# Kernel optimization log

Hardware: AMD Instinct MI355X
Metric: run time of the kernel (lower is better)

## Reference

```python
import jax, jax.numpy as jnp
import numpy as np

N_NODES = 50000
N_EDGES = 800000
NODE_IN, EDGE_IN, EFT, OUT = 128, 64, 32, 64


def setup_inputs() -> dict:
    key = jax.random.key(0)
    ks = jax.random.split(key, 8)
    h = jax.random.normal(ks[0], (N_NODES, NODE_IN), dtype=jnp.float32)
    edge_feat = jax.random.normal(ks[1], (N_EDGES, EDGE_IN), dtype=jnp.float32)
    src = jax.random.randint(ks[2], (N_EDGES,), 0, N_NODES, dtype=jnp.int32)
    dst = jax.random.randint(ks[3], (N_EDGES,), 0, N_NODES, dtype=jnp.int32)
    Wn = jax.random.normal(ks[4], (OUT, NODE_IN), dtype=jnp.float32) * 0.05
    We = jax.random.normal(ks[5], (EFT, EDGE_IN), dtype=jnp.float32) * 0.05
    Wa = jax.random.normal(ks[6], (1, OUT + EFT + OUT), dtype=jnp.float32) * 0.05
    W2 = jax.random.normal(ks[7], (OUT, OUT + EFT), dtype=jnp.float32) * 0.05
    return {"h": h, "edge_feat": edge_feat, "src": src, "dst": dst,
            "Wn": Wn, "We": We, "Wa": Wa, "W2": W2}


def reference(h, edge_feat, src, dst, Wn, We, Wa, W2):
    N = h.shape[0]
    # node / edge feature projections (bias=False linears)
    z = h @ Wn.T                       # [N, OUT]
    ef = edge_feat @ We.T              # [E, EFT]
    # per-edge message: concat(src node ft, edge ft)
    zne = jnp.concatenate([z[src], ef], axis=1)            # [E, OUT+EFT]
    # attention logit: leaky_relu(attn_fc([zne, z_dst]))
    a = jnp.concatenate([zne, z[dst]], axis=1) @ Wa.T      # [E, 1]
    s = jax.nn.leaky_relu(a[:, 0], negative_slope=0.01)    # [E]
    # segment softmax over incoming edges of each dst node
    seg_max = jax.ops.segment_max(s, dst, num_segments=N)
    ex = jnp.exp(s - seg_max[dst])
    denom = jax.ops.segment_sum(ex, dst, num_segments=N)
    alpha = ex / denom[dst]                                # [E]
    # weighted scatter-sum aggregation, then fc2
    agg = jax.ops.segment_sum(alpha[:, None] * zne, dst, num_segments=N)
    h_new = agg @ W2.T                                     # [N, OUT]
    # DGL semantics: nodes with no incoming messages keep ndata['z'] = fc_n(h)
    deg = jax.ops.segment_sum(jnp.ones_like(s), dst, num_segments=N)
    return jnp.where((deg > 0)[:, None], h_new, z)
```

## Files before the change

### kernel.cpp

```cpp
#include <hip/hip_runtime.h>
#include <hip/hip_bf16.h>
#include <math.h>

#define N_NODES 50000
#define N_EDGES 800000
#define NB1 196

typedef __attribute__((ext_vector_type(8))) short bf16x8;
typedef __attribute__((ext_vector_type(4))) float f32x4;

__device__ __forceinline__ unsigned short f2bf(float f) {
    union { __hip_bfloat16 b; unsigned short u; } cv;
    cv.b = __float2bfloat16(f);
    return cv.u;
}
__device__ __forceinline__ float bf2f(unsigned short u) {
    return __uint_as_float(((unsigned)u) << 16);
}
__device__ __forceinline__ unsigned pack2bf(float a, float b) {
    return (unsigned)f2bf(a) | ((unsigned)f2bf(b) << 16);
}
union BFU { bf16x8 v; unsigned u[4]; };

__global__ __launch_bounds__(256) void kw_kernel(const float* __restrict__ We,
                                                 const float* __restrict__ Wa,
                                                 const float* __restrict__ Wn,
                                                 const float* __restrict__ W2,
                                                 short* __restrict__ Bpack,
                                                 int* __restrict__ degi) {
    int t = blockIdx.x * 256 + threadIdx.x;
    if (t < N_NODES) degi[t] = 0;
    if (t < 34 * 512) {
        int f = t >> 9, u = t & 511, lane = u >> 3, j = u & 7;
        int c = lane & 15, G = lane >> 4;
        float v = 0.f;
        if (f < 8) {
            int s = f >> 2, n = f & 3;
            int kp = 32 * s + 8 * G + j;
            #pragma unroll
            for (int kk = 0; kk < 32; ++kk)
                v += W2[(16 * n + c) * 96 + 64 + kk] * We[kk * 64 + kp];
        } else if (f < 10) {
            int s = f - 8;
            if (c == 0) {
                int kp = 32 * s + 8 * G + j;
                #pragma unroll
                for (int jj = 0; jj < 32; ++jj) v += Wa[64 + jj] * We[jj * 64 + kp];
            }
        } else if (f < 26) {
            int qf = f - 10, s = qf >> 2, n = qf & 3;
            v = Wn[(16 * n + c) * 128 + 32 * s + 8 * G + j];
        } else {
            int qf = f - 26, s = qf >> 2, n = qf & 3;
            v = W2[(16 * n + c) * 96 + 32 * s + 8 * G + j];
        }
        Bpack[t] = (short)f2bf(v);
    }
}

__global__ __launch_bounds__(256) void node_hist_kernel(
    const float* __restrict__ h, const float* __restrict__ Wa,
    const short* __restrict__ Bpack, const int* __restrict__ dst,
    float* __restrict__ z, ushort4* __restrict__ y16p,
    float* __restrict__ asrc, float* __restrict__ adst,
    int* __restrict__ degi, int* __restrict__ ranks)
{
    __shared__ float zl[4][1088];
    int t = threadIdx.x;
    if (blockIdx.x >= 782) {
        int e = (blockIdx.x - 782) * 256 + t;
        if (e < N_EDGES) ranks[e] = atomicAdd(&degi[dst[e]], 1);
        return;
    }
    int w = t >> 6, l = t & 63, c = l & 15, G = l >> 4;
    int T = blockIdx.x * 4 + w;
    if (T >= 3125) return;
    int n0 = T * 16;
    const bf16x8* Bp = (const bf16x8*)Bpack;

    const float* hp = h + (size_t)(n0 + c) * 128 + 8 * G;
    bf16x8 a[4];
    #pragma unroll
    for (int s = 0; s < 4; ++s) {
        float4 lo = *(const float4*)(hp + 32 * s);
        float4 hi = *(const float4*)(hp + 32 * s + 4);
        BFU ua;
        ua.u[0] = pack2bf(lo.x, lo.y);
        ua.u[1] = pack2bf(lo.z, lo.w);
        ua.u[2] = pack2bf(hi.x, hi.y);
        ua.u[3] = pack2bf(hi.z, hi.w);
        a[s] = ua.v;
    }
    f32x4 acc[4] = {{0.f,0.f,0.f,0.f},{0.f,0.f,0.f,0.f},{0.f,0.f,0.f,0.f},{0.f,0.f,0.f,0.f}};
    #pragma unroll
    for (int n = 0; n < 4; ++n)
        #pragma unroll
        for (int s = 0; s < 4; ++s)
            acc[n] = __builtin_amdgcn_mfma_f32_16x16x32_bf16(a[s], Bp[(10 + 4*s + n)*64 + l], acc[n], 0, 0, 0);

    float was[4], wad[4];
    #pragma unroll
    for (int n = 0; n < 4; ++n) { was[n] = Wa[16*n + c]; wad[n] = Wa[96 + 16*n + c]; }

    #pragma unroll
    for (int r = 0; r < 4; ++r) {
        int row = n0 + 4 * G + r;
        #pragma unroll
        for (int n = 0; n < 4; ++n) {
            z[(size_t)row * 64 + 16 * n + c] = acc[n][r];
            zl[w][(4 * G + r) * 68 + 16 * n + c] = acc[n][r];
        }
        float ps = acc[0][r]*was[0] + acc[1][r]*was[1] + acc[2][r]*was[2] + acc[3][r]*was[3];
        float pd = acc[0][r]*wad[0] + acc[1][r]*wad[1] + acc[2][r]*wad[2] + acc[3][r]*wad[3];
        ps += __shfl_xor(ps, 1); ps += __shfl_xor(ps, 2);
        ps += __shfl_xor(ps, 4); ps += __shfl_xor(ps, 8);
        pd += __shfl_xor(pd, 1); pd += __shfl_xor(pd, 2);
        pd += __shfl_xor(pd, 4); pd += __shfl_xor(pd, 8);
        if (c == 0) { asrc[row] = ps; adst[row] = pd; }
    }

    bf16x8 ay[2];
    #pragma unroll
    for (int s = 0; s < 2; ++s) {
        BFU ua;
        #pragma unroll
        for (int jp = 0; jp < 4; ++jp)
            ua.u[jp] = pack2bf(zl[w][c * 68 + 32 * s + 8 * G + 2 * jp],
                               zl[w][c * 68 + 32 * s + 8 * G + 2 * jp + 1]);
        ay[s] = ua.v;
    }
    f32x4 accy[4] = {{0.f,0.f,0.f,0.f},{0.f,0.f,0.f,0.f},{0.f,0.f,0.f,0.f},{0.f,0.f,0.f,0.f}};
    #pragma unroll
    for (int n = 0; n < 4; ++n)
        #pragma unroll
        for (int s = 0; s < 2; ++s)
            accy[n] = __builtin_amdgcn_mfma_f32_16x16x32_bf16(ay[s], Bp[(26 + 4*s + n)*64 + l], accy[n], 0, 0, 0);
    #pragma unroll
    for (int r = 0; r < 4; ++r) {
        ushort4 yo;
        yo.x = f2bf(accy[0][r]); yo.y = f2bf(accy[1][r]);
        yo.z = f2bf(accy[2][r]); yo.w = f2bf(accy[3][r]);
        y16p[(size_t)(n0 + 4 * G + r) * 16 + c] = yo;
    }
}

__global__ __launch_bounds__(256) void scan1_kernel(const int* __restrict__ degi,
                                                    int* __restrict__ partial) {
    int t = threadIdx.x, i = blockIdx.x * 256 + t;
    int d = (i < N_NODES) ? degi[i] : 0;
    #pragma unroll
    for (int off = 32; off; off >>= 1) d += __shfl_down(d, off);
    __shared__ int wsum[4];
    if ((t & 63) == 0) wsum[t >> 6] = d;
    __syncthreads();
    if (t == 0) partial[blockIdx.x] = wsum[0] + wsum[1] + wsum[2] + wsum[3];
}

__global__ __launch_bounds__(256) void scan2_kernel(int* __restrict__ partial) {
    __shared__ int s[256];
    int t = threadIdx.x;
    int v = (t < NB1) ? partial[t] : 0;
    s[t] = v; __syncthreads();
    for (int off = 1; off < 256; off <<= 1) {
        int x = (t >= off) ? s[t - off] : 0;
        __syncthreads();
        s[t] += x;
        __syncthreads();
    }
    if (t < NB1) partial[t] = s[t] - v;
}

__global__ __launch_bounds__(256) void scan3_kernel(const int* __restrict__ degi,
                                                    const int* __restrict__ partial,
                                                    int* __restrict__ start) {
    __shared__ int s[256];
    int t = threadIdx.x, i = blockIdx.x * 256 + t;
    int d = (i < N_NODES) ? degi[i] : 0;
    s[t] = d; __syncthreads();
    for (int off = 1; off < 256; off <<= 1) {
        int x = (t >= off) ? s[t - off] : 0;
        __syncthreads();
        s[t] += x;
        __syncthreads();
    }
    if (i < N_NODES) start[i] = partial[blockIdx.x] + s[t] - d;
}

__global__ __launch_bounds__(256, 2) void edge_kernel(
    const float* __restrict__ edge_feat, const int* __restrict__ src,
    const int* __restrict__ dst, const int* __restrict__ ranks,
    const int* __restrict__ start, const float* __restrict__ asrc,
    const float* __restrict__ adst, const short* __restrict__ Bpack,
    const ushort4* __restrict__ y16p,
    unsigned short* __restrict__ wout, float* __restrict__ exslot)
{
    int t = threadIdx.x, w = t >> 6, l = t & 63;
    int c = l & 15, G = l >> 4;
    int wbase = blockIdx.x * 256 + w * 64;

    const bf16x8* Bp = (const bf16x8*)Bpack;
    bf16x8 bc[8];
    #pragma unroll
    for (int f = 0; f < 8; ++f) bc[f] = Bp[f * 64 + l];
    bf16x8 b2a = Bp[8 * 64 + l];
    bf16x8 b2b = Bp[9 * 64 + l];

    int e = wbase + l;
    int se = src[e];
    int de = dst[e];
    int slot = start[de] + ranks[e];
    float apre = asrc[se] + adst[de];

    const float* efr = edge_feat + (size_t)(wbase + c) * 64 + G * 8;
    float4 n0 = *(const float4*)(efr);
    float4 n1 = *(const float4*)(efr + 4);
    float4 n2 = *(const float4*)(efr + 32);
    float4 n3 = *(const float4*)(efr + 36);

    #pragma unroll
    for (int k = 0; k < 4; ++k) {
        float4 c0 = n0, c1 = n1, c2 = n2, c3 = n3;
        if (k < 3) {
            const float* efn = edge_feat + (size_t)(wbase + 16 * (k + 1) + c) * 64 + G * 8;
            n0 = *(const float4*)(efn);
            n1 = *(const float4*)(efn + 4);
            n2 = *(const float4*)(efn + 32);
            n3 = *(const float4*)(efn + 36);
        }
        int sr[4], sl4[4]; float ap[4];
        #pragma unroll
        for (int r = 0; r < 4; ++r) {
            int si = 16 * k + 4 * G + r;
            sr[r]  = __shfl(se, si);
            sl4[r] = __shfl(slot, si);
            ap[r]  = __shfl(apre, si);
        }
        ushort4 yv[4];
        #pragma unroll
        for (int r = 0; r < 4; ++r) yv[r] = y16p[(size_t)sr[r] * 16 + c];

        BFU ua0, ua1;
        ua0.u[0] = pack2bf(c0.x, c0.y);
        ua0.u[1] = pack2bf(c0.z, c0.w);
        ua0.u[2] = pack2bf(c1.x, c1.y);
        ua0.u[3] = pack2bf(c1.z, c1.w);
        ua1.u[0] = pack2bf(c2.x, c2.y);
        ua1.u[1] = pack2bf(c2.z, c2.w);
        ua1.u[2] = pack2bf(c3.x, c3.y);
        ua1.u[3] = pack2bf(c3.z, c3.w);
        bf16x8 a0 = ua0.v, a1 = ua1.v;

        f32x4 acc[4] = {{0.f,0.f,0.f,0.f},{0.f,0.f,0.f,0.f},{0.f,0.f,0.f,0.f},{0.f,0.f,0.f,0.f}};
        f32x4 acc2 = {0.f, 0.f, 0.f, 0.f};
        #pragma unroll
        for (int n = 0; n < 4; ++n) {
            acc[n] = __builtin_amdgcn_mfma_f32_16x16x32_bf16(a0, bc[n], acc[n], 0, 0, 0);
            acc[n] = __builtin_amdgcn_mfma_f32_16x16x32_bf16(a1, bc[4 + n], acc[n], 0, 0, 0);
        }
        acc2 = __builtin_amdgcn_mfma_f32_16x16x32_bf16(a0, b2a, acc2, 0, 0, 0);
        acc2 = __builtin_amdgcn_mfma_f32_16x16x32_bf16(a1, b2b, acc2, 0, 0, 0);

        #pragma unroll
        for (int r = 0; r < 4; ++r) {
            float u0 = acc[0][r] + bf2f(yv[r].x);
            float u1 = acc[1][r] + bf2f(yv[r].y);
            float u2 = acc[2][r] + bf2f(yv[r].z);
            float u3 = acc[3][r] + bf2f(yv[r].w);
            uint2 o;
            o.x = pack2bf(u0, u1);
            o.y = pack2bf(u2, u3);
            *(uint2*)&wout[(size_t)sl4[r] * 64 + 4 * c] = o;
            if (c == 0) {
                float aa = ap[r] + acc2[r];
                float sg = aa > 0.f ? aa : 0.01f * aa;
                exslot[sl4[r]] = __expf(sg);
            }
        }
    }
}

__global__ __launch_bounds__(256) void agg_kernel(
    const ushort4* __restrict__ wout4, const float* __restrict__ exslot,
    const int* __restrict__ start, const int* __restrict__ degi,
    const float* __restrict__ z, float* __restrict__ out)
{
    int t = threadIdx.x, w = t >> 6, l = t & 63, c = l & 15, g = l >> 4;
    int d    = blockIdx.x * 4 + w;
    int base = __builtin_amdgcn_readfirstlane(start[d]);
    int deg  = __builtin_amdgcn_readfirstlane(degi[d]);

    float4 acc = make_float4(0.f, 0.f, 0.f, 0.f);
    float den = 0.f;
    for (int i = 0; i < deg; i += 8) {
        int i0 = i + g, i1 = i + 4 + g;
        bool v0 = i0 < deg, v1 = i1 < deg;
        int k0 = v0 ? i0 : 0, k1 = v1 ? i1 : 0;
        ushort4 ua = wout4[(size_t)(base + k0) * 16 + c];
        ushort4 ub = wout4[(size_t)(base + k1) * 16 + c];
        float xa = v0 ? exslot[base + i0] : 0.f;
        float xb = v1 ? exslot[base + i1] : 0.f;
        acc.x += xa * bf2f(ua.x); acc.y += xa * bf2f(ua.y);
        acc.z += xa * bf2f(ua.z); acc.w += xa * bf2f(ua.w);
        den += xa;
        acc.x += xb * bf2f(ub.x); acc.y += xb * bf2f(ub.y);
        acc.z += xb * bf2f(ub.z); acc.w += xb * bf2f(ub.w);
        den += xb;
    }

    acc.x += __shfl_xor(acc.x, 16); acc.x += __shfl_xor(acc.x, 32);
    acc.y += __shfl_xor(acc.y, 16); acc.y += __shfl_xor(acc.y, 32);
    acc.z += __shfl_xor(acc.z, 16); acc.z += __shfl_xor(acc.z, 32);
    acc.w += __shfl_xor(acc.w, 16); acc.w += __shfl_xor(acc.w, 32);
    den += __shfl_xor(den, 16); den += __shfl_xor(den, 32);

    if (g == 0) {
        size_t ob = (size_t)d * 64;
        if (deg > 0) {
            float inv = 1.f / den;
            out[ob + c]      = acc.x * inv;
            out[ob + 16 + c] = acc.y * inv;
            out[ob + 32 + c] = acc.z * inv;
            out[ob + 48 + c] = acc.w * inv;
        } else {
            out[ob + c]      = z[ob + c];
            out[ob + 16 + c] = z[ob + 16 + c];
            out[ob + 32 + c] = z[ob + 32 + c];
            out[ob + 48 + c] = z[ob + 48 + c];
        }
    }
}

extern "C" void kernel_launch(void* const* d_in, const int* in_sizes, int n_in,
                              void* d_out, int out_size, void* d_ws, size_t ws_size,
                              hipStream_t stream) {
    const float* h         = (const float*)d_in[0];
    const float* edge_feat = (const float*)d_in[1];
    const int*   src       = (const int*)d_in[2];
    const int*   dst       = (const int*)d_in[3];
    const float* Wn        = (const float*)d_in[4];
    const float* We        = (const float*)d_in[5];
    const float* Wa        = (const float*)d_in[6];
    const float* W2        = (const float*)d_in[7];
    float* out = (float*)d_out;

    char* p = (char*)d_ws;
    unsigned short* wout   = (unsigned short*)p; p += (size_t)N_EDGES * 64 * 2;
    float*          z      = (float*)p;          p += (size_t)N_NODES * 64 * 4;
    ushort4*        y16p   = (ushort4*)p;        p += (size_t)N_NODES * 64 * 2;
    float*          exslot = (float*)p;          p += (size_t)N_EDGES * 4;
    float*          asrc   = (float*)p;          p += (size_t)N_NODES * 4;
    float*          adst   = (float*)p;          p += (size_t)N_NODES * 4;
    int*            degi   = (int*)p;            p += (size_t)N_NODES * 4;
    int*            start  = (int*)p;            p += (size_t)N_NODES * 4;
    int*            ranks  = (int*)p;            p += (size_t)N_EDGES * 4;
    int*            partial= (int*)p;            p += (size_t)256 * 4;
    short*          Bpack  = (short*)p;          p += (size_t)34 * 512 * 2;

    kw_kernel<<<NB1, 256, 0, stream>>>(We, Wa, Wn, W2, Bpack, degi);
    node_hist_kernel<<<782 + 3125, 256, 0, stream>>>(h, Wa, Bpack, dst, z, y16p,
                                                     asrc, adst, degi, ranks);
    scan1_kernel<<<NB1, 256, 0, stream>>>(degi, partial);
    scan2_kernel<<<1, 256, 0, stream>>>(partial);
    scan3_kernel<<<NB1, 256, 0, stream>>>(degi, partial, start);
    edge_kernel<<<3125, 256, 0, stream>>>(edge_feat, src, dst, ranks, start,
                                          asrc, adst, Bpack, y16p, wout, exslot);
    agg_kernel<<<N_NODES / 4, 256, 0, stream>>>((const ushort4*)wout, exslot,
                                                start, degi, z, out);
}
```

Before: 168.6 us.

## Process one 16-edge tile per wave in edge kernel, raise occupancy

Each wave now handles 16 edges in a single MFMA tile instead of looping over four 16-edge tiles with software-prefetched edge features. The grid grows to N_EDGES/64 blocks and launch bounds ask for 4 blocks per CU, so more waves can hide gather and scatter latency. In exchange, each wave still loads the full B-matrix fragments into registers for a quarter of the work, only 16 of 64 lanes load indices, and the explicit prefetch pipelining is gone.

```diff
diff --git a/kernel.cpp b/kernel.cpp
--- a/kernel.cpp
+++ b/kernel.cpp
@@ -186,7 +186,7 @@
     if (i < N_NODES) start[i] = partial[blockIdx.x] + s[t] - d;
 }
 
-__global__ __launch_bounds__(256, 2) void edge_kernel(
+__global__ __launch_bounds__(256, 4) void edge_kernel(
     const float* __restrict__ edge_feat, const int* __restrict__ src,
     const int* __restrict__ dst, const int* __restrict__ ranks,
     const int* __restrict__ start, const float* __restrict__ asrc,
@@ -196,7 +196,7 @@
 {
     int t = threadIdx.x, w = t >> 6, l = t & 63;
     int c = l & 15, G = l >> 4;
-    int wbase = blockIdx.x * 256 + w * 64;
+    int wbase = blockIdx.x * 64 + w * 16;
 
     const bf16x8* Bp = (const bf16x8*)Bpack;
     bf16x8 bc[8];
@@ -205,76 +205,68 @@
     bf16x8 b2a = Bp[8 * 64 + l];
     bf16x8 b2b = Bp[9 * 64 + l];
 
-    int e = wbase + l;
-    int se = src[e];
-    int de = dst[e];
-    int slot = start[de] + ranks[e];
-    float apre = asrc[se] + adst[de];
+    int se = 0, slot = 0; float apre = 0.f;
+    if (l < 16) {
+        int e = wbase + l;
+        se = src[e];
+        int de = dst[e];
+        slot = start[de] + ranks[e];
+        apre = asrc[se] + adst[de];
+    }
 
     const float* efr = edge_feat + (size_t)(wbase + c) * 64 + G * 8;
-    float4 n0 = *(const float4*)(efr);
-    float4 n1 = *(const float4*)(efr + 4);
-    float4 n2 = *(const float4*)(efr + 32);
-    float4 n3 = *(const float4*)(efr + 36);
-
-    #pragma unroll
-    for (int k = 0; k < 4; ++k) {
-        float4 c0 = n0, c1 = n1, c2 = n2, c3 = n3;
-        if (k < 3) {
-            const float* efn = edge_feat + (size_t)(wbase + 16 * (k + 1) + c) * 64 + G * 8;
-            n0 = *(const float4*)(efn);
-            n1 = *(const float4*)(efn + 4);
-            n2 = *(const float4*)(efn + 32);
-            n3 = *(const float4*)(efn + 36);
-        }
-        int sr[4], sl4[4]; float ap[4];
-        #pragma unroll
-        for (int r = 0; r < 4; ++r) {
-            int si = 16 * k + 4 * G + r;
-            sr[r]  = __shfl(se, si);
-            sl4[r] = __shfl(slot, si);
-            ap[r]  = __shfl(apre, si);
-        }
-        ushort4 yv[4];
-        #pragma unroll
-        for (int r = 0; r < 4; ++r) yv[r] = y16p[(size_t)sr[r] * 16 + c];
-
-        BFU ua0, ua1;
-        ua0.u[0] = pack2bf(c0.x, c0.y);
-        ua0.u[1] = pack2bf(c0.z, c0.w);
-        ua0.u[2] = pack2bf(c1.x, c1.y);
-        ua0.u[3] = pack2bf(c1.z, c1.w);
-        ua1.u[0] = pack2bf(c2.x, c2.y);
-        ua1.u[1] = pack2bf(c2.z, c2.w);
-        ua1.u[2] = pack2bf(c3.x, c3.y);
-        ua1.u[3] = pack2bf(c3.z, c3.w);
-        bf16x8 a0 = ua0.v, a1 = ua1.v;
-
-        f32x4 acc[4] = {{0.f,0.f,0.f,0.f},{0.f,0.f,0.f,0.f},{0.f,0.f,0.f,0.f},{0.f,0.f,0.f,0.f}};
-        f32x4 acc2 = {0.f, 0.f, 0.f, 0.f};
-        #pragma unroll
-        for (int n = 0; n < 4; ++n) {
-            acc[n] = __builtin_amdgcn_mfma_f32_16x16x32_bf16(a0, bc[n], acc[n], 0, 0, 0);
-            acc[n] = __builtin_amdgcn_mfma_f32_16x16x32_bf16(a1, bc[4 + n], acc[n], 0, 0, 0);
-        }
-        acc2 = __builtin_amdgcn_mfma_f32_16x16x32_bf16(a0, b2a, acc2, 0, 0, 0);
-        acc2 = __builtin_amdgcn_mfma_f32_16x16x32_bf16(a1, b2b, acc2, 0, 0, 0);
-
-        #pragma unroll
-        for (int r = 0; r < 4; ++r) {
-            float u0 = acc[0][r] + bf2f(yv[r].x);
-            float u1 = acc[1][r] + bf2f(yv[r].y);
-            float u2 = acc[2][r] + bf2f(yv[r].z);
-            float u3 = acc[3][r] + bf2f(yv[r].w);
-            uint2 o;
-            o.x = pack2bf(u0, u1);
-            o.y = pack2bf(u2, u3);
-            *(uint2*)&wout[(size_t)sl4[r] * 64 + 4 * c] = o;
-            if (c == 0) {
-                float aa = ap[r] + acc2[r];
-                float sg = aa > 0.f ? aa : 0.01f * aa;
-                exslot[sl4[r]] = __expf(sg);
-            }
+    float4 c0 = *(const float4*)(efr);
+    float4 c1 = *(const float4*)(efr + 4);
+    float4 c2 = *(const float4*)(efr + 32);
+    float4 c3 = *(const float4*)(efr + 36);
+
+    int sr[4], sl4[4]; float ap[4];
+    #pragma unroll
+    for (int r = 0; r < 4; ++r) {
+        int si = 4 * G + r;
+        sr[r]  = __shfl(se, si);
+        sl4[r] = __shfl(slot, si);
+        ap[r]  = __shfl(apre, si);
+    }
+    ushort4 yv[4];
+    #pragma unroll
+    for (int r = 0; r < 4; ++r) yv[r] = y16p[(size_t)sr[r] * 16 + c];
+
+    BFU ua0, ua1;
+    ua0.u[0] = pack2bf(c0.x, c0.y);
+    ua0.u[1] = pack2bf(c0.z, c0.w);
+    ua0.u[2] = pack2bf(c1.x, c1.y);
+    ua0.u[3] = pack2bf(c1.z, c1.w);
+    ua1.u[0] = pack2bf(c2.x, c2.y);
+    ua1.u[1] = pack2bf(c2.z, c2.w);
+    ua1.u[2] = pack2bf(c3.x, c3.y);
+    ua1.u[3] = pack2bf(c3.z, c3.w);
+    bf16x8 a0 = ua0.v, a1 = ua1.v;
+
+    f32x4 acc[4] = {{0.f,0.f,0.f,0.f},{0.f,0.f,0.f,0.f},{0.f,0.f,0.f,0.f},{0.f,0.f,0.f,0.f}};
+    f32x4 acc2 = {0.f, 0.f, 0.f, 0.f};
+    #pragma unroll
+    for (int n = 0; n < 4; ++n) {
+        acc[n] = __builtin_amdgcn_mfma_f32_16x16x32_bf16(a0, bc[n], acc[n], 0, 0, 0);
+        acc[n] = __builtin_amdgcn_mfma_f32_16x16x32_bf16(a1, bc[4 + n], acc[n], 0, 0, 0);
+    }
+    acc2 = __builtin_amdgcn_mfma_f32_16x16x32_bf16(a0, b2a, acc2, 0, 0, 0);
+    acc2 = __builtin_amdgcn_mfma_f32_16x16x32_bf16(a1, b2b, acc2, 0, 0, 0);
+
+    #pragma unroll
+    for (int r = 0; r < 4; ++r) {
+        float u0 = acc[0][r] + bf2f(yv[r].x);
+        float u1 = acc[1][r] + bf2f(yv[r].y);
+        float u2 = acc[2][r] + bf2f(yv[r].z);
+        float u3 = acc[3][r] + bf2f(yv[r].w);
+        uint2 o;
+        o.x = pack2bf(u0, u1);
+        o.y = pack2bf(u2, u3);
+        *(uint2*)&wout[(size_t)sl4[r] * 64 + 4 * c] = o;
+        if (c == 0) {
+            float aa = ap[r] + acc2[r];
+            float sg = aa > 0.f ? aa : 0.01f * aa;
+            exslot[sl4[r]] = __expf(sg);
         }
     }
 }
@@ -362,8 +354,8 @@
     scan1_kernel<<<NB1, 256, 0, stream>>>(degi, partial);
     scan2_kernel<<<1, 256, 0, stream>>>(partial);
     scan3_kernel<<<NB1, 256, 0, stream>>>(degi, partial, start);
-    edge_kernel<<<3125, 256, 0, stream>>>(edge_feat, src, dst, ranks, start,
-                                          asrc, adst, Bpack, y16p, wout, exslot);
+    edge_kernel<<<N_EDGES / 64, 256, 0, stream>>>(edge_feat, src, dst, ranks, start,
+                                                  asrc, adst, Bpack, y16p, wout, exslot);
     agg_kernel<<<N_NODES / 4, 256, 0, stream>>>((const ushort4*)wout, exslot,
                                                 start, degi, z, out);
 }
```

After: 189.5 us. 12.4% more time.
